# Kernel optimization log

Measured on AMD Instinct MI355X. Metric: run time of the kernel, lower is better.

The kernel has to match this reference:

```python
import jax, jax.numpy as jnp
import numpy as np

KERNEL_SIZE = 15
PAD = (KERNEL_SIZE - 1) // 2


def _dark_channel(x):
    # x: [B, 3, H, W] in [-1, 1]
    x = (x + 1.0) / 2.0
    x = jnp.min(x, axis=1, keepdims=True)            # channel min -> [B,1,H,W]
    x = jnp.pad(x, ((0, 0), (0, 0), (PAD, PAD), (PAD, PAD)), mode='reflect')
    # sliding-window min (morphological erosion), VALID after reflect pad
    x = jax.lax.reduce_window(
        x, jnp.inf, jax.lax.min,
        window_dimensions=(1, 1, KERNEL_SIZE, KERNEL_SIZE),
        window_strides=(1, 1, 1, 1),
        padding='VALID')
    return jnp.clip(x, 0.0, 0.1)


def setup_inputs() -> dict:
    key = jax.random.key(0)
    k1, k2 = jax.random.split(key)
    shape = (16, 3, 512, 512)
    # tanh-range images in [-1, 1]
    real = jax.random.uniform(k1, shape, dtype=jnp.float32) * 2.0 - 1.0
    fake = jax.random.uniform(k2, shape, dtype=jnp.float32) * 2.0 - 1.0
    return {"real": real, "fake": fake}


def reference(real, fake):
    real_map = _dark_channel(real)
    fake_map = _dark_channel(fake)
    diff = real_map - fake_map
    return jnp.mean(diff * diff)  # nn.MSELoss (mean reduction)
```

## Files before the change

### kernel.cpp

```cpp
#include <hip/hip_runtime.h>

#define BDIM 256
#define TILE 64
#define HALO 7
#define IN_T 78
#define CSTR 84
#define VSTR 82
#define IMG 512
#define HW (IMG * IMG)
#define NPIX (16.0f * 512.0f * 512.0f)
#define P1_TASKS (IN_T * 20)
#define NBLK 1024

typedef float f4 __attribute__((ext_vector_type(4)));

__device__ __forceinline__ int reflect_idx(int i, int n) {
    i = (i < 0) ? -i : i;
    i = (i >= n) ? (2 * n - 2 - i) : i;
    return i;
}

__device__ __forceinline__ unsigned short umin16(unsigned short a, unsigned short b) {
    return a < b ? a : b;
}

__device__ __forceinline__ unsigned short map_bf16(float v) {
    float m = fminf(fmaxf(fmaf(v, 0.5f, 0.5f), 0.0f), 0.1f);
    unsigned int u = __float_as_uint(m);
    return (unsigned short)((u + 0x7fffu + ((u >> 16) & 1u)) >> 16);
}

__device__ __forceinline__ float bf16_f32(unsigned short x) {
    return __uint_as_float(((unsigned int)x) << 16);
}

__device__ __forceinline__ void phase2(const unsigned short* __restrict__ cm,
                                       unsigned short* __restrict__ vm, int tid) {
    #pragma unroll
    for (int b = 0; b < 2; ++b) {
        int t = tid + b * BDIM;
        if (t < IN_T * 4) {
            int col = (unsigned)t % (unsigned)IN_T;
            int rr0 = ((unsigned)t / (unsigned)IN_T) * 16;
            const unsigned short* cp = cm + (col + 1);
            unsigned short s[15];
            #pragma unroll
            for (int j = 0; j < 15; ++j) s[j] = cp[(rr0 + j) * CSTR];
            #pragma unroll
            for (int j = 13; j >= 0; --j) s[j] = umin16(s[j], s[j + 1]);
            unsigned short* vp = vm + col;
            vp[rr0 * VSTR] = s[0];
            unsigned short f = cp[(rr0 + 15) * CSTR];
            #pragma unroll
            for (int i2 = 1; i2 <= 14; ++i2) {
                vp[(rr0 + i2) * VSTR] = umin16(s[i2], f);
                f = umin16(f, cp[(rr0 + 15 + i2) * CSTR]);
            }
            vp[(rr0 + 15) * VSTR] = f;
        }
    }
}

__device__ __forceinline__ void phase3(const unsigned short* __restrict__ vm,
                                       int tid, float (&o)[16]) {
    int row = tid >> 2, k = tid & 3;
    const unsigned int* vr = (const unsigned int*)(vm + row * VSTR) + 8 * k;
    unsigned short x[32];
    #pragma unroll
    for (int j = 0; j < 16; ++j) {
        unsigned int d = vr[j];
        x[2 * j] = (unsigned short)d;
        x[2 * j + 1] = (unsigned short)(d >> 16);
    }
    unsigned short s[15];
    #pragma unroll
    for (int j = 0; j < 15; ++j) s[j] = x[j];
    #pragma unroll
    for (int j = 13; j >= 0; --j) s[j] = umin16(s[j], s[j + 1]);
    o[0] = bf16_f32(s[0]);
    unsigned short f = x[15];
    #pragma unroll
    for (int i2 = 1; i2 <= 14; ++i2) {
        o[i2] = bf16_f32(umin16(s[i2], f));
        f = umin16(f, x[15 + i2]);
    }
    o[15] = bf16_f32(f);
}

__global__ __launch_bounds__(BDIM, 4)
void dcl_kernel(const float* __restrict__ real, const float* __restrict__ fake,
                float* __restrict__ ws) {
    __shared__ __align__(8) unsigned short cmr[IN_T * CSTR];
    __shared__ __align__(8) unsigned short cmf[IN_T * CSTR];
    __shared__ __align__(8) unsigned short vm[TILE * VSTR];
    __shared__ float red[BDIM / 64];

    const int tid = threadIdx.x;
    const int bid = blockIdx.x;
    const int xcd = bid & 7;
    const int s_ = bid >> 3;
    const int z  = s_ & 15;
    const int tt = s_ >> 4;
    const int bx = (xcd & 1) * 4 + (tt & 3);
    const int by = (xcd >> 1) * 2 + (tt >> 2);

    const int r0g = by * TILE - HALO;
    const int c0g = bx * TILE - HALO;
    const bool fastcol = (bx >= 1) && (bx <= 6);
    const size_t ib = (size_t)z * 3 * HW;
    const float* __restrict__ Rb = real + ib;
    const float* __restrict__ Fb = fake + ib;

    f4 bR[2][3], bF[2][3];

    auto load_i = [&](int i, f4 (&R3)[3], f4 (&F3)[3]) {
        int t = tid + i * BDIM;
        t = t < (P1_TASKS - 1) ? t : (P1_TASKS - 1);
        int row = (unsigned)t / 20u;
        int g = t - row * 20;
        int gr = reflect_idx(r0g + row, IMG);
        const float* rpR = Rb + (size_t)gr * IMG;
        const float* rpF = Fb + (size_t)gr * IMG;
        if (fastcol) {
            const float* pR = rpR + (c0g - 1 + 4 * g);
            const float* pF = rpF + (c0g - 1 + 4 * g);
            R3[0] = *(const f4*)pR;
            R3[1] = *(const f4*)(pR + HW);
            R3[2] = *(const f4*)(pR + 2 * HW);
            F3[0] = *(const f4*)pF;
            F3[1] = *(const f4*)(pF + HW);
            F3[2] = *(const f4*)(pF + 2 * HW);
        } else {
            #pragma unroll
            for (int k = 0; k < 4; ++k) {
                int gc = reflect_idx(c0g - 1 + 4 * g + k, IMG);
                R3[0][k] = rpR[gc]; R3[1][k] = rpR[HW + gc]; R3[2][k] = rpR[2 * HW + gc];
                F3[0][k] = rpF[gc]; F3[1][k] = rpF[HW + gc]; F3[2][k] = rpF[2 * HW + gc];
            }
        }
    };

    auto consume_i = [&](int i, const f4 (&R3)[3], const f4 (&F3)[3]) {
        int t = tid + i * BDIM;
        t = t < (P1_TASKS - 1) ? t : (P1_TASKS - 1);
        int row = (unsigned)t / 20u;
        int g = t - row * 20;
        unsigned short wr[4], wf[4];
        #pragma unroll
        for (int k = 0; k < 4; ++k) {
            wr[k] = map_bf16(fminf(R3[0][k], fminf(R3[1][k], R3[2][k])));
            wf[k] = map_bf16(fminf(F3[0][k], fminf(F3[1][k], F3[2][k])));
        }
        uint2 pr, pf;
        pr.x = (unsigned)wr[0] | ((unsigned)wr[1] << 16);
        pr.y = (unsigned)wr[2] | ((unsigned)wr[3] << 16);
        pf.x = (unsigned)wf[0] | ((unsigned)wf[1] << 16);
        pf.y = (unsigned)wf[2] | ((unsigned)wf[3] << 16);
        *(uint2*)&cmr[row * CSTR + 4 * g] = pr;
        *(uint2*)&cmf[row * CSTR + 4 * g] = pf;
    };

    load_i(0, bR[0], bF[0]);
    #pragma unroll
    for (int i = 0; i < 7; ++i) {
        if (i < 6) load_i(i + 1, bR[(i + 1) & 1], bF[(i + 1) & 1]);
        consume_i(i, bR[i & 1], bF[i & 1]);
    }
    __syncthreads();

    float o_r[16], o_f[16];
    phase2(cmr, vm, tid);
    __syncthreads();
    phase3(vm, tid, o_r);
    __syncthreads();
    phase2(cmf, vm, tid);
    __syncthreads();
    phase3(vm, tid, o_f);

    float acc = 0.f;
    #pragma unroll
    for (int i = 0; i < 16; ++i) {
        float d = o_r[i] - o_f[i];
        acc += d * d;
    }
    #pragma unroll
    for (int off = 32; off >= 1; off >>= 1)
        acc += __shfl_xor(acc, off, 64);
    if ((tid & 63) == 0) red[tid >> 6] = acc;
    __syncthreads();
    if (tid == 0)
        ws[bid] = red[0] + red[1] + red[2] + red[3];
}

__global__ __launch_bounds__(256)
void reduce_kernel(const float* __restrict__ ws, float* __restrict__ out) {
    __shared__ float red[4];
    int tid = threadIdx.x;
    float a = ws[tid] + ws[tid + 256] + ws[tid + 512] + ws[tid + 768];
    #pragma unroll
    for (int off = 32; off >= 1; off >>= 1)
        a += __shfl_xor(a, off, 64);
    if ((tid & 63) == 0) red[tid >> 6] = a;
    __syncthreads();
    if (tid == 0)
        out[0] = (red[0] + red[1] + red[2] + red[3]) * (1.0f / NPIX);
}

extern "C" void kernel_launch(void* const* d_in, const int* in_sizes, int n_in,
                              void* d_out, int out_size, void* d_ws, size_t ws_size,
                              hipStream_t stream) {
    const float* real = (const float*)d_in[0];
    const float* fake = (const float*)d_in[1];
    float* ws = (float*)d_ws;
    float* out = (float*)d_out;
    dcl_kernel<<<dim3(NBLK), BDIM, 0, stream>>>(real, fake, ws);
    reduce_kernel<<<1, 256, 0, stream>>>(ws, out);
}
```

Baseline: 132.8 us.

## Use 64x32 tiles with more blocks and drop manual load double-buffering

Halves the tile height to 32 rows, which doubles the grid to 2048 blocks. The launch bound is raised to 8 blocks per CU and the block-to-tile mapping is remapped across XCDs. The explicit register double-buffered load loop is replaced by a simple unrolled loop, and the vertical and horizontal min passes now use only part of the threads. The aim is higher occupancy and more latency hiding through extra resident blocks. In exchange, the halo overhead per output pixel grows (46 input rows for 32 output rows instead of 78 for 64), and half the threads sit idle in the later phases.

```diff
diff --git a/kernel.cpp b/kernel.cpp
--- a/kernel.cpp
+++ b/kernel.cpp
@@ -1,16 +1,17 @@
 #include <hip/hip_runtime.h>
 
 #define BDIM 256
-#define TILE 64
+#define TILE_W 64
+#define TILE_H 32
 #define HALO 7
-#define IN_T 78
-#define CSTR 84
+#define IN_R 46
+#define CSTR 80
 #define VSTR 82
 #define IMG 512
 #define HW (IMG * IMG)
 #define NPIX (16.0f * 512.0f * 512.0f)
-#define P1_TASKS (IN_T * 20)
-#define NBLK 1024
+#define P1_TASKS (IN_R * 20)
+#define NBLK 2048
 
 typedef float f4 __attribute__((ext_vector_type(4)));
 
@@ -36,28 +37,24 @@
 
 __device__ __forceinline__ void phase2(const unsigned short* __restrict__ cm,
                                        unsigned short* __restrict__ vm, int tid) {
-    #pragma unroll
-    for (int b = 0; b < 2; ++b) {
-        int t = tid + b * BDIM;
-        if (t < IN_T * 4) {
-            int col = (unsigned)t % (unsigned)IN_T;
-            int rr0 = ((unsigned)t / (unsigned)IN_T) * 16;
-            const unsigned short* cp = cm + (col + 1);
-            unsigned short s[15];
-            #pragma unroll
-            for (int j = 0; j < 15; ++j) s[j] = cp[(rr0 + j) * CSTR];
-            #pragma unroll
-            for (int j = 13; j >= 0; --j) s[j] = umin16(s[j], s[j + 1]);
-            unsigned short* vp = vm + col;
-            vp[rr0 * VSTR] = s[0];
-            unsigned short f = cp[(rr0 + 15) * CSTR];
-            #pragma unroll
-            for (int i2 = 1; i2 <= 14; ++i2) {
-                vp[(rr0 + i2) * VSTR] = umin16(s[i2], f);
-                f = umin16(f, cp[(rr0 + 15 + i2) * CSTR]);
-            }
-            vp[(rr0 + 15) * VSTR] = f;
-        }
+    if (tid < 78 * 2) {
+        int col = (unsigned)tid % 78u;
+        int rr0 = ((unsigned)tid / 78u) * 16;
+        const unsigned short* cp = cm + (col + 1);
+        unsigned short s[15];
+        #pragma unroll
+        for (int j = 0; j < 15; ++j) s[j] = cp[(rr0 + j) * CSTR];
+        #pragma unroll
+        for (int j = 13; j >= 0; --j) s[j] = umin16(s[j], s[j + 1]);
+        unsigned short* vp = vm + col;
+        vp[rr0 * VSTR] = s[0];
+        unsigned short f = cp[(rr0 + 15) * CSTR];
+        #pragma unroll
+        for (int i2 = 1; i2 <= 14; ++i2) {
+            vp[(rr0 + i2) * VSTR] = umin16(s[i2], f);
+            f = umin16(f, cp[(rr0 + 15 + i2) * CSTR]);
+        }
+        vp[(rr0 + 15) * VSTR] = f;
     }
 }
 
@@ -87,33 +84,32 @@
     o[15] = bf16_f32(f);
 }
 
-__global__ __launch_bounds__(BDIM, 4)
+__global__ __launch_bounds__(BDIM, 8)
 void dcl_kernel(const float* __restrict__ real, const float* __restrict__ fake,
                 float* __restrict__ ws) {
-    __shared__ __align__(8) unsigned short cmr[IN_T * CSTR];
-    __shared__ __align__(8) unsigned short cmf[IN_T * CSTR];
-    __shared__ __align__(8) unsigned short vm[TILE * VSTR];
+    __shared__ __align__(8) unsigned short cmr[IN_R * CSTR];
+    __shared__ __align__(8) unsigned short cmf[IN_R * CSTR];
+    __shared__ __align__(8) unsigned short vm[TILE_H * VSTR];
     __shared__ float red[BDIM / 64];
 
     const int tid = threadIdx.x;
     const int bid = blockIdx.x;
     const int xcd = bid & 7;
-    const int s_ = bid >> 3;
-    const int z  = s_ & 15;
-    const int tt = s_ >> 4;
-    const int bx = (xcd & 1) * 4 + (tt & 3);
-    const int by = (xcd >> 1) * 2 + (tt >> 2);
-
-    const int r0g = by * TILE - HALO;
-    const int c0g = bx * TILE - HALO;
+    const int r_ = bid >> 3;
+    const int z  = r_ >> 4;
+    const int p  = r_ & 15;
+    const int bx = (xcd & 3) * 2 + (p & 1);
+    const int by = (xcd >> 2) * 8 + (p >> 1);
+
+    const int r0g = by * TILE_H - HALO;
+    const int c0g = bx * TILE_W - HALO;
     const bool fastcol = (bx >= 1) && (bx <= 6);
     const size_t ib = (size_t)z * 3 * HW;
     const float* __restrict__ Rb = real + ib;
     const float* __restrict__ Fb = fake + ib;
 
-    f4 bR[2][3], bF[2][3];
-
-    auto load_i = [&](int i, f4 (&R3)[3], f4 (&F3)[3]) {
+    #pragma unroll
+    for (int i = 0; i < 4; ++i) {
         int t = tid + i * BDIM;
         t = t < (P1_TASKS - 1) ? t : (P1_TASKS - 1);
         int row = (unsigned)t / 20u;
@@ -121,6 +117,7 @@
         int gr = reflect_idx(r0g + row, IMG);
         const float* rpR = Rb + (size_t)gr * IMG;
         const float* rpF = Fb + (size_t)gr * IMG;
+        f4 R3[3], F3[3];
         if (fastcol) {
             const float* pR = rpR + (c0g - 1 + 4 * g);
             const float* pF = rpF + (c0g - 1 + 4 * g);
@@ -138,13 +135,6 @@
                 F3[0][k] = rpF[gc]; F3[1][k] = rpF[HW + gc]; F3[2][k] = rpF[2 * HW + gc];
             }
         }
-    };
-
-    auto consume_i = [&](int i, const f4 (&R3)[3], const f4 (&F3)[3]) {
-        int t = tid + i * BDIM;
-        t = t < (P1_TASKS - 1) ? t : (P1_TASKS - 1);
-        int row = (unsigned)t / 20u;
-        int g = t - row * 20;
         unsigned short wr[4], wf[4];
         #pragma unroll
         for (int k = 0; k < 4; ++k) {
@@ -158,30 +148,25 @@
         pf.y = (unsigned)wf[2] | ((unsigned)wf[3] << 16);
         *(uint2*)&cmr[row * CSTR + 4 * g] = pr;
         *(uint2*)&cmf[row * CSTR + 4 * g] = pf;
-    };
-
-    load_i(0, bR[0], bF[0]);
-    #pragma unroll
-    for (int i = 0; i < 7; ++i) {
-        if (i < 6) load_i(i + 1, bR[(i + 1) & 1], bF[(i + 1) & 1]);
-        consume_i(i, bR[i & 1], bF[i & 1]);
     }
     __syncthreads();
 
     float o_r[16], o_f[16];
     phase2(cmr, vm, tid);
     __syncthreads();
-    phase3(vm, tid, o_r);
+    if (tid < 128) phase3(vm, tid, o_r);
     __syncthreads();
     phase2(cmf, vm, tid);
     __syncthreads();
-    phase3(vm, tid, o_f);
+    if (tid < 128) phase3(vm, tid, o_f);
 
     float acc = 0.f;
-    #pragma unroll
-    for (int i = 0; i < 16; ++i) {
-        float d = o_r[i] - o_f[i];
-        acc += d * d;
+    if (tid < 128) {
+        #pragma unroll
+        for (int i = 0; i < 16; ++i) {
+            float d = o_r[i] - o_f[i];
+            acc += d * d;
+        }
     }
     #pragma unroll
     for (int off = 32; off >= 1; off >>= 1)
@@ -196,7 +181,9 @@
 void reduce_kernel(const float* __restrict__ ws, float* __restrict__ out) {
     __shared__ float red[4];
     int tid = threadIdx.x;
-    float a = ws[tid] + ws[tid + 256] + ws[tid + 512] + ws[tid + 768];
+    float a = 0.f;
+    #pragma unroll
+    for (int j = 0; j < 8; ++j) a += ws[tid + 256 * j];
     #pragma unroll
     for (int off = 32; off >= 1; off >>= 1)
         a += __shfl_xor(a, off, 64);
```

Measured after the change: 148.0 us. 1.11x slower.

## Split channel-min mapping into separate pass writing bf16 maps to workspace

Applied to the files above, without the earlier changes.

Adds a map_kernel that reads the full fp32 inputs once, computes the clipped channel-min, and writes compact bf16 maps to workspace. The tile kernel then loads these 16-bit maps with the halo, so overlapping halo rows cost 2-byte reads instead of three 4-byte channel reads. The trade-off is an extra kernel launch plus a global write and re-read of the intermediate maps. The old fused kernel is kept as a fallback when the workspace is too small, with its software double-buffered load loop removed.

```diff
diff --git a/kernel.cpp b/kernel.cpp
--- a/kernel.cpp
+++ b/kernel.cpp
@@ -1,16 +1,19 @@
 #include <hip/hip_runtime.h>
 
+#define IMG 512
+#define HW (IMG * IMG)
+#define NPIX (16.0f * 512.0f * 512.0f)
+
+#define ABLK 2048
 #define BDIM 256
 #define TILE 64
 #define HALO 7
 #define IN_T 78
-#define CSTR 84
+#define CSTR 88
 #define VSTR 82
-#define IMG 512
-#define HW (IMG * IMG)
-#define NPIX (16.0f * 512.0f * 512.0f)
-#define P1_TASKS (IN_T * 20)
-#define NBLK 1024
+#define NBLK_B 1024
+#define FCSTR 84
+#define F_P1T (IN_T * 20)
 
 typedef float f4 __attribute__((ext_vector_type(4)));
 
@@ -19,19 +22,49 @@
     i = (i >= n) ? (2 * n - 2 - i) : i;
     return i;
 }
-
 __device__ __forceinline__ unsigned short umin16(unsigned short a, unsigned short b) {
     return a < b ? a : b;
 }
-
 __device__ __forceinline__ unsigned short map_bf16(float v) {
     float m = fminf(fmaxf(fmaf(v, 0.5f, 0.5f), 0.0f), 0.1f);
     unsigned int u = __float_as_uint(m);
     return (unsigned short)((u + 0x7fffu + ((u >> 16) & 1u)) >> 16);
 }
-
 __device__ __forceinline__ float bf16_f32(unsigned short x) {
     return __uint_as_float(((unsigned int)x) << 16);
+}
+
+__global__ __launch_bounds__(256)
+void map_kernel(const float* __restrict__ real, const float* __restrict__ fake,
+                unsigned short* __restrict__ cmr, unsigned short* __restrict__ cmf) {
+    int i0 = blockIdx.x * 256 + threadIdx.x;
+    #pragma unroll
+    for (int u = 0; u < 2; ++u) {
+        int i = i0 + u * 524288;
+        int z = i >> 16;
+        int p = (i & 65535) << 2;
+        const float* pr = real + (size_t)z * 3 * HW + p;
+        const float* pf = fake + (size_t)z * 3 * HW + p;
+        f4 r0 = *(const f4*)pr;
+        f4 r1 = *(const f4*)(pr + HW);
+        f4 r2 = *(const f4*)(pr + 2 * HW);
+        f4 f0 = *(const f4*)pf;
+        f4 f1 = *(const f4*)(pf + HW);
+        f4 f2 = *(const f4*)(pf + 2 * HW);
+        unsigned short wr[4], wf[4];
+        #pragma unroll
+        for (int k = 0; k < 4; ++k) {
+            wr[k] = map_bf16(fminf(r0[k], fminf(r1[k], r2[k])));
+            wf[k] = map_bf16(fminf(f0[k], fminf(f1[k], f2[k])));
+        }
+        uint2 ur, uf;
+        ur.x = (unsigned)wr[0] | ((unsigned)wr[1] << 16);
+        ur.y = (unsigned)wr[2] | ((unsigned)wr[3] << 16);
+        uf.x = (unsigned)wf[0] | ((unsigned)wf[1] << 16);
+        uf.y = (unsigned)wf[2] | ((unsigned)wf[3] << 16);
+        *(uint2*)(cmr + (size_t)z * HW + p) = ur;
+        *(uint2*)(cmf + (size_t)z * HW + p) = uf;
+    }
 }
 
 __device__ __forceinline__ void phase2(const unsigned short* __restrict__ cm,
@@ -87,11 +120,12 @@
     o[15] = bf16_f32(f);
 }
 
-__global__ __launch_bounds__(BDIM, 4)
-void dcl_kernel(const float* __restrict__ real, const float* __restrict__ fake,
-                float* __restrict__ ws) {
-    __shared__ __align__(8) unsigned short cmr[IN_T * CSTR];
-    __shared__ __align__(8) unsigned short cmf[IN_T * CSTR];
+__global__ __launch_bounds__(BDIM)
+void dcl_tile(const unsigned short* __restrict__ cmr_g,
+              const unsigned short* __restrict__ cmf_g,
+              float* __restrict__ ws) {
+    __shared__ __align__(16) unsigned short cmr[IN_T * CSTR];
+    __shared__ __align__(16) unsigned short cmf[IN_T * CSTR];
     __shared__ __align__(8) unsigned short vm[TILE * VSTR];
     __shared__ float red[BDIM / 64];
 
@@ -99,7 +133,80 @@
     const int bid = blockIdx.x;
     const int xcd = bid & 7;
     const int s_ = bid >> 3;
-    const int z  = s_ & 15;
+    const int z = s_ & 15;
+    const int tt = s_ >> 4;
+    const int bx = (xcd & 1) * 4 + (tt & 3);
+    const int by = (xcd >> 1) * 2 + (tt >> 2);
+
+    const int r0g = by * TILE - HALO;
+    const int c0g = bx * TILE - HALO;
+    const bool fastcol = (bx >= 1) && (bx <= 6);
+    const unsigned short* br = cmr_g + (size_t)z * HW;
+    const unsigned short* bf = cmf_g + (size_t)z * HW;
+
+    #pragma unroll
+    for (int it = 0; it < 4; ++it) {
+        int t = tid + it * BDIM;
+        t = t < 779 ? t : 779;
+        int row = (unsigned)t / 10u;
+        int g = t - row * 10;
+        int gr = reflect_idx(r0g + row, IMG);
+        const unsigned short* rr = br + (size_t)gr * IMG;
+        const unsigned short* rf = bf + (size_t)gr * IMG;
+        if (fastcol) {
+            int gc = c0g - 1 + 8 * g;
+            uint4 qr = *(const uint4*)(rr + gc);
+            uint4 qf = *(const uint4*)(rf + gc);
+            *(uint4*)&cmr[row * CSTR + 8 * g] = qr;
+            *(uint4*)&cmf[row * CSTR + 8 * g] = qf;
+        } else {
+            #pragma unroll
+            for (int k = 0; k < 8; ++k) {
+                int gc = reflect_idx(c0g - 1 + 8 * g + k, IMG);
+                cmr[row * CSTR + 8 * g + k] = rr[gc];
+                cmf[row * CSTR + 8 * g + k] = rf[gc];
+            }
+        }
+    }
+    __syncthreads();
+
+    float o_r[16], o_f[16];
+    phase2(cmr, vm, tid);
+    __syncthreads();
+    phase3(vm, tid, o_r);
+    __syncthreads();
+    phase2(cmf, vm, tid);
+    __syncthreads();
+    phase3(vm, tid, o_f);
+
+    float acc = 0.f;
+    #pragma unroll
+    for (int i = 0; i < 16; ++i) {
+        float d = o_r[i] - o_f[i];
+        acc += d * d;
+    }
+    #pragma unroll
+    for (int off = 32; off >= 1; off >>= 1)
+        acc += __shfl_xor(acc, off, 64);
+    if ((tid & 63) == 0) red[tid >> 6] = acc;
+    __syncthreads();
+    if (tid == 0)
+        ws[bid] = red[0] + red[1] + red[2] + red[3];
+}
+
+__global__ __launch_bounds__(BDIM, 4)
+void dcl_fused(const float* __restrict__ real, const float* __restrict__ fake,
+               float* __restrict__ ws) {
+    __shared__ __align__(8) unsigned short cmr[IN_T * FCSTR];
+    __shared__ __align__(8) unsigned short cmf[IN_T * FCSTR];
+    __shared__ __align__(8) unsigned short vmf[TILE * VSTR];
+    __shared__ float red[BDIM / 64];
+
+    const int tid = threadIdx.x;
+    const int bid = blockIdx.x;
+    const int xcd = bid & 7;
+    const int s_ = bid >> 3;
+    const int z = s_ & 15;
     const int tt = s_ >> 4;
     const int bx = (xcd & 1) * 4 + (tt & 3);
     const int by = (xcd >> 1) * 2 + (tt >> 2);
@@ -111,25 +218,21 @@
     const float* __restrict__ Rb = real + ib;
     const float* __restrict__ Fb = fake + ib;
 
-    f4 bR[2][3], bF[2][3];
-
-    auto load_i = [&](int i, f4 (&R3)[3], f4 (&F3)[3]) {
+    #pragma unroll
+    for (int i = 0; i < 7; ++i) {
         int t = tid + i * BDIM;
-        t = t < (P1_TASKS - 1) ? t : (P1_TASKS - 1);
+        t = t < (F_P1T - 1) ? t : (F_P1T - 1);
         int row = (unsigned)t / 20u;
         int g = t - row * 20;
         int gr = reflect_idx(r0g + row, IMG);
         const float* rpR = Rb + (size_t)gr * IMG;
         const float* rpF = Fb + (size_t)gr * IMG;
+        f4 R3[3], F3[3];
         if (fastcol) {
             const float* pR = rpR + (c0g - 1 + 4 * g);
             const float* pF = rpF + (c0g - 1 + 4 * g);
-            R3[0] = *(const f4*)pR;
-            R3[1] = *(const f4*)(pR + HW);
-            R3[2] = *(const f4*)(pR + 2 * HW);
-            F3[0] = *(const f4*)pF;
-            F3[1] = *(const f4*)(pF + HW);
-            F3[2] = *(const f4*)(pF + 2 * HW);
+            R3[0] = *(const f4*)pR; R3[1] = *(const f4*)(pR + HW); R3[2] = *(const f4*)(pR + 2 * HW);
+            F3[0] = *(const f4*)pF; F3[1] = *(const f4*)(pF + HW); F3[2] = *(const f4*)(pF + 2 * HW);
         } else {
             #pragma unroll
             for (int k = 0; k < 4; ++k) {
@@ -138,13 +241,6 @@
                 F3[0][k] = rpF[gc]; F3[1][k] = rpF[HW + gc]; F3[2][k] = rpF[2 * HW + gc];
             }
         }
-    };
-
-    auto consume_i = [&](int i, const f4 (&R3)[3], const f4 (&F3)[3]) {
-        int t = tid + i * BDIM;
-        t = t < (P1_TASKS - 1) ? t : (P1_TASKS - 1);
-        int row = (unsigned)t / 20u;
-        int g = t - row * 20;
         unsigned short wr[4], wf[4];
         #pragma unroll
         for (int k = 0; k < 4; ++k) {
@@ -156,26 +252,63 @@
         pr.y = (unsigned)wr[2] | ((unsigned)wr[3] << 16);
         pf.x = (unsigned)wf[0] | ((unsigned)wf[1] << 16);
         pf.y = (unsigned)wf[2] | ((unsigned)wf[3] << 16);
-        *(uint2*)&cmr[row * CSTR + 4 * g] = pr;
-        *(uint2*)&cmf[row * CSTR + 4 * g] = pf;
-    };
-
-    load_i(0, bR[0], bF[0]);
-    #pragma unroll
-    for (int i = 0; i < 7; ++i) {
-        if (i < 6) load_i(i + 1, bR[(i + 1) & 1], bF[(i + 1) & 1]);
-        consume_i(i, bR[i & 1], bF[i & 1]);
+        *(uint2*)&cmr[row * FCSTR + 4 * g] = pr;
+        *(uint2*)&cmf[row * FCSTR + 4 * g] = pf;
     }
     __syncthreads();
 
     float o_r[16], o_f[16];
-    phase2(cmr, vm, tid);
-    __syncthreads();
-    phase3(vm, tid, o_r);
-    __syncthreads();
-    phase2(cmf, vm, tid);
-    __syncthreads();
-    phase3(vm, tid, o_f);
+    #pragma unroll
+    for (int b = 0; b < 2; ++b) {
+        int t = tid + b * BDIM;
+        if (t < IN_T * 4) {
+            int col = (unsigned)t % (unsigned)IN_T;
+            int rr0 = ((unsigned)t / (unsigned)IN_T) * 16;
+            const unsigned short* cp = cmr + (col + 1);
+            unsigned short s[15];
+            #pragma unroll
+            for (int j = 0; j < 15; ++j) s[j] = cp[(rr0 + j) * FCSTR];
+            #pragma unroll
+            for (int j = 13; j >= 0; --j) s[j] = umin16(s[j], s[j + 1]);
+            unsigned short* vp = vmf + col;
+            vp[rr0 * VSTR] = s[0];
+            unsigned short f = cp[(rr0 + 15) * FCSTR];
+            #pragma unroll
+            for (int i2 = 1; i2 <= 14; ++i2) {
+                vp[(rr0 + i2) * VSTR] = umin16(s[i2], f);
+                f = umin16(f, cp[(rr0 + 15 + i2) * FCSTR]);
+            }
+            vp[(rr0 + 15) * VSTR] = f;
+        }
+    }
+    __syncthreads();
+    phase3(vmf, tid, o_r);
+    __syncthreads();
+    #pragma unroll
+    for (int b = 0; b < 2; ++b) {
+        int t = tid + b * BDIM;
+        if (t < IN_T * 4) {
+            int col = (unsigned)t % (unsigned)IN_T;
+            int rr0 = ((unsigned)t / (unsigned)IN_T) * 16;
+            const unsigned short* cp = cmf + (col + 1);
+            unsigned short s[15];
+            #pragma unroll
+            for (int j = 0; j < 15; ++j) s[j] = cp[(rr0 + j) * FCSTR];
+            #pragma unroll
+            for (int j = 13; j >= 0; --j) s[j] = umin16(s[j], s[j + 1]);
+            unsigned short* vp = vmf + col;
+            vp[rr0 * VSTR] = s[0];
+            unsigned short f = cp[(rr0 + 15) * FCSTR];
+            #pragma unroll
+            for (int i2 = 1; i2 <= 14; ++i2) {
+                vp[(rr0 + i2) * VSTR] = umin16(s[i2], f);
+                f = umin16(f, cp[(rr0 + 15 + i2) * FCSTR]);
+            }
+            vp[(rr0 + 15) * VSTR] = f;
+        }
+    }
+    __syncthreads();
+    phase3(vmf, tid, o_f);
 
     float acc = 0.f;
     #pragma unroll
@@ -213,6 +346,16 @@
     const float* fake = (const float*)d_in[1];
     float* ws = (float*)d_ws;
     float* out = (float*)d_out;
-    dcl_kernel<<<dim3(NBLK), BDIM, 0, stream>>>(real, fake, ws);
+
+    const size_t cm_bytes = (size_t)16 * HW * 2;
+    const size_t need = 8192 + 2 * cm_bytes;
+    if (ws_size >= need) {
+        unsigned short* cmr = (unsigned short*)((char*)d_ws + 8192);
+        unsigned short* cmf = (unsigned short*)((char*)d_ws + 8192 + cm_bytes);
+        map_kernel<<<dim3(ABLK), 256, 0, stream>>>(real, fake, cmr, cmf);
+        dcl_tile<<<dim3(NBLK_B), BDIM, 0, stream>>>(cmr, cmf, ws);
+    } else {
+        dcl_fused<<<dim3(NBLK_B), BDIM, 0, stream>>>(real, fake, ws);
+    }
     reduce_kernel<<<1, 256, 0, stream>>>(ws, out);
 }
```

Measured after the change: 126.3 us. 1.05x faster.
